# Kernel optimization log

Measured on AMD Instinct MI355X. Metric: run time of the kernel, lower is better.

Reference implementation:

```python
import jax, jax.numpy as jnp
import numpy as np

EPS = float(jnp.finfo(jnp.float32).eps)


def _mlp(x, W1, b1, W2, b2, W3, b3):
    h = jax.nn.relu(x @ W1 + b1)
    h = jax.nn.relu(h @ W2 + b2)
    return h @ W3 + b3


def setup_inputs() -> dict:
    B, D_A, D_B, K, H = 131072, 16, 16, 32, 256
    key = jax.random.key(0)
    ks = jax.random.split(key, 13)
    def lin(k, fi, fo):
        return jax.random.normal(k, (fi, fo), jnp.float32) * (fi ** -0.5)
    inp = {
        "x": jax.random.uniform(ks[0], (B, D_A + D_B), jnp.float32),
        "hW1": lin(ks[1], D_A, H), "hb1": jnp.zeros((H,), jnp.float32),
        "hW2": lin(ks[2], H, H),   "hb2": jnp.zeros((H,), jnp.float32),
        "hW3": lin(ks[3], H, D_B * (K + 1)), "hb3": jnp.zeros((D_B * (K + 1),), jnp.float32),
        "wW1": lin(ks[4], D_A, H), "wb1": jnp.zeros((H,), jnp.float32),
        "wW2": lin(ks[5], H, H),   "wb2": jnp.zeros((H,), jnp.float32),
        "wW3": lin(ks[6], H, D_B * K), "wb3": jnp.zeros((D_B * K,), jnp.float32),
        "A_dims": jnp.arange(0, 32, 2, dtype=jnp.int32),
        "B_dims": jnp.arange(1, 32, 2, dtype=jnp.int32),
    }
    return inp


def reference(x, hW1, hb1, hW2, hb2, hW3, hb3, wW1, wb1, wW2, wb2, wW3, wb3, A_dims, B_dims):
    B = x.shape[0]
    D_B = B_dims.shape[0]
    K = wW3.shape[1] // D_B
    x_A = x[:, A_dims]               # (B, D_A)
    x_B = x[:, B_dims]               # (B, D_B)

    raw_h = _mlp(x_A, hW1, hb1, hW2, hb2, hW3, hb3).reshape(B, D_B, K + 1)
    heights = jax.nn.softplus(raw_h) + EPS
    raw_w = _mlp(x_A, wW1, wb1, wW2, wb2, wW3, wb3).reshape(B, D_B, K)
    widths = jax.nn.softmax(raw_w, axis=-1)
    zeros = jnp.zeros((B, D_B, 1), x.dtype)
    bins = jnp.concatenate([zeros, jnp.cumsum(widths, axis=-1)], axis=-1)  # (B, D_B, K+1)

    # preprocess_params_2: normalise PDF heights and bin areas
    bin_widths = bins[:, :, 1:] - bins[:, :, :-1]
    bin_areas = 0.5 * (heights[:, :, :-1] + heights[:, :, 1:]) * bin_widths  # (B, D_B, K)
    total_area = bin_areas.sum(axis=-1, keepdims=True)
    v = heights / total_area
    bin_areas = bin_areas / total_area

    # bin search
    i = jnp.sum(x_B[..., None] >= bins, axis=-1) - 1
    i = jnp.clip(i, 0, K - 1)                                  # (B, D_B)
    iu = i[..., None]

    x_left = jnp.take_along_axis(bins, iu, axis=2)[..., 0]
    x_right = jnp.take_along_axis(bins, iu + 1, axis=2)[..., 0]
    w_b = x_right - x_left
    v_left = jnp.take_along_axis(v, iu, axis=2)[..., 0]
    v_right = jnp.take_along_axis(v, iu + 1, axis=2)[..., 0]
    w_v = v_right - v_left

    alpha = (x_B - x_left) / (w_b + EPS)
    # cumulative area up to left edge of bin i: exclusive prefix sum then gather
    c_edges = jnp.concatenate([zeros, jnp.cumsum(bin_areas, axis=-1)], axis=-1)
    c_left = jnp.take_along_axis(c_edges, iu, axis=2)[..., 0]

    y_B = c_left + 0.5 * alpha ** 2 * w_v * w_b + alpha * v_left * w_b
    y = x.at[:, B_dims].set(y_B)
    return y
```

## Files before the change

kernel.cpp:

```cpp
#include <hip/hip_runtime.h>
#include <cmath>

typedef short short8 __attribute__((ext_vector_type(8)));
typedef float f32x16 __attribute__((ext_vector_type(16)));

#define EPSF 1.1920929e-07f

#define LDS_XA  0
#define LDS_A1H 3072
#define LDS_A1W 36864
#define LDS_A2H 70656
#define LDS_A2W 104448
#define LDS_H32 3072
#define LDS_TOTAL 138240

#define OFF1H 0
#define OFF1W 4096
#define OFF2H 8192
#define OFF2W 73728
#define OFF3W 139264
#define OFF3H 270336
#define OFFH32 401408

__device__ __forceinline__ unsigned short f2bf(float f) {
  union { float f; unsigned u; } v; v.f = f;
  return (unsigned short)((v.u + 0x8000u) >> 16);
}
__device__ __forceinline__ float sp_eps(float v) {
  return fmaxf(v, 0.f) + __logf(1.f + __expf(-fabsf(v))) + EPSF;
}
__device__ __forceinline__ int chanm(int m) {
  return (((m >> 2) & 1) << 4) + (m & 3) + ((m >> 3) << 2);
}

__global__ void pack_weights(const float* __restrict__ hW1, const float* __restrict__ wW1,
                             const float* __restrict__ hW2, const float* __restrict__ wW2,
                             const float* __restrict__ hW3, const float* __restrict__ wW3,
                             unsigned short* __restrict__ out) {
  int bid = blockIdx.x, l = threadIdx.x;
  int m = l & 31;
  const float* W; unsigned short* dst; int tile, col, NC;
  if (bid < 8)        { W = hW1; dst = out + OFF1H;  tile = bid;       col = tile * 32 + chanm(m); NC = 256; }
  else if (bid < 16)  { W = wW1; dst = out + OFF1W;  tile = bid - 8;   col = tile * 32 + chanm(m); NC = 256; }
  else if (bid < 144) { W = hW2; dst = out + OFF2H;  tile = bid - 16;  col = (tile >> 4) * 32 + chanm(m); NC = 256; }
  else if (bid < 272) { W = wW2; dst = out + OFF2W;  tile = bid - 144; col = (tile >> 4) * 32 + chanm(m); NC = 256; }
  else if (bid < 528) { W = wW3; dst = out + OFF3W;  tile = bid - 272; col = (tile >> 4) * 32 + chanm(m); NC = 512; }
  else if (bid < 784) { W = hW3; dst = out + OFF3H;  tile = bid - 528; col = (tile >> 4) * 33 + chanm(m); NC = 528; }
  else {
    W = hW3; dst = out + OFFH32; tile = bid - 784;
    int q = (m >> 2) & 1, rr = (m & 3) + ((m >> 3) << 2);
    col = q ? -1 : rr * 33 + 32; NC = 528;
  }
  int kt = (bid < 16) ? 0 : (tile & 15);
  int K  = (bid < 16) ? 16 : 256;
  int k0 = kt * 16 + (l >> 5) * 8;
  short8 v;
  #pragma unroll
  for (int e = 0; e < 8; e++) {
    float f = (col >= 0 && (k0 + e) < K) ? W[(k0 + e) * NC + col] : 0.f;
    v[e] = (short)f2bf(f);
  }
  *(short8*)(dst + (tile * 64 + l) * 8) = v;
}

__device__ __forceinline__ void store_relu16(unsigned short* dstRow, f32x16 a) {
  uint4 p0, p1;
  unsigned pk[8];
  #pragma unroll
  for (int j = 0; j < 8; j++) {
    unsigned lo = f2bf(fmaxf(a[2 * j], 0.f));
    unsigned hi = f2bf(fmaxf(a[2 * j + 1], 0.f));
    pk[j] = lo | (hi << 16);
  }
  p0.x = pk[0]; p0.y = pk[1]; p0.z = pk[2]; p0.w = pk[3];
  p1.x = pk[4]; p1.y = pk[5]; p1.z = pk[6]; p1.w = pk[7];
  *(uint4*)(dstRow) = p0;
  *(uint4*)(dstRow + 8) = p1;
}

__global__ __launch_bounds__(1024, 4) void fused_kernel(
    const float* __restrict__ x,
    const float* __restrict__ hb1, const float* __restrict__ hb2, const float* __restrict__ hb3,
    const float* __restrict__ wb1, const float* __restrict__ wb2, const float* __restrict__ wb3,
    const unsigned short* __restrict__ pw,
    float* __restrict__ y) {
  extern __shared__ char lds[];
  const int t = threadIdx.x;
  const int w = t >> 6, l = t & 63, q = l >> 5, r32 = l & 31;
  const int r0 = blockIdx.x * 64;

  unsigned short* XA  = (unsigned short*)(lds + LDS_XA);
  unsigned short* A1H = (unsigned short*)(lds + LDS_A1H);
  unsigned short* A1W = (unsigned short*)(lds + LDS_A1W);
  unsigned short* A2H = (unsigned short*)(lds + LDS_A2H);
  unsigned short* A2W = (unsigned short*)(lds + LDS_A2W);
  float* H32 = (float*)(lds + LDS_H32);

  if (t < 512) {
    int row = t >> 3, c4 = t & 7;
    float4 v = *(const float4*)(x + (r0 + row) * 32 + c4 * 4);
    y[(r0 + row) * 32 + c4 * 4] = v.x;
    y[(r0 + row) * 32 + c4 * 4 + 2] = v.z;
    unsigned short* xa = XA + row * 24 + c4 * 2;
    xa[0] = f2bf(v.x); xa[1] = f2bf(v.z);
  }
  __syncthreads();

  const int net = w >> 3, tc = w & 7;
  unsigned short* A1n = net ? A1W : A1H;
  unsigned short* A2n = net ? A2W : A2H;

  {
    const unsigned short* pA = pw + (net ? OFF1W : OFF1H) + tc * 512;
    const float* b1 = net ? wb1 : hb1;
    f32x16 a0, a1;
    #pragma unroll
    for (int rr = 0; rr < 16; rr++) { float bv = b1[tc * 32 + q * 16 + rr]; a0[rr] = bv; a1[rr] = bv; }
    short8 af = *(const short8*)(pA + l * 8);
    short8 b0 = *(const short8*)(XA + r32 * 24 + q * 8);
    short8 b1f = *(const short8*)(XA + (32 + r32) * 24 + q * 8);
    a0 = __builtin_amdgcn_mfma_f32_32x32x16_bf16(af, b0, a0, 0, 0, 0);
    a1 = __builtin_amdgcn_mfma_f32_32x32x16_bf16(af, b1f, a1, 0, 0, 0);
    store_relu16(A1n + r32 * 264 + tc * 32 + q * 16, a0);
    store_relu16(A1n + (32 + r32) * 264 + tc * 32 + q * 16, a1);
  }
  __syncthreads();

  {
    const unsigned short* pA = pw + (net ? OFF2W : OFF2H) + tc * 16 * 512;
    const float* b2 = net ? wb2 : hb2;
    f32x16 a0, a1;
    #pragma unroll
    for (int rr = 0; rr < 16; rr++) { float bv = b2[tc * 32 + q * 16 + rr]; a0[rr] = bv; a1[rr] = bv; }
    #pragma unroll
    for (int kt = 0; kt < 16; kt++) {
      short8 af = *(const short8*)(pA + kt * 512 + l * 8);
      short8 b0 = *(const short8*)(A1n + r32 * 264 + kt * 16 + q * 8);
      short8 b1f = *(const short8*)(A1n + (32 + r32) * 264 + kt * 16 + q * 8);
      a0 = __builtin_amdgcn_mfma_f32_32x32x16_bf16(af, b0, a0, 0, 0, 0);
      a1 = __builtin_amdgcn_mfma_f32_32x32x16_bf16(af, b1f, a1, 0, 0, 0);
    }
    store_relu16(A2n + r32 * 264 + tc * 32 + q * 16, a0);
    store_relu16(A2n + (32 + r32) * 264 + tc * 32 + q * 16, a1);
  }
  __syncthreads();

  const int d = w;
  f32x16 ew0, ew1, hh0, hh1;
  #pragma unroll
  for (int rr = 0; rr < 16; rr++) {
    float wv = wb3[d * 32 + q * 16 + rr];
    float hv = hb3[d * 33 + q * 16 + rr];
    ew0[rr] = wv; ew1[rr] = wv; hh0[rr] = hv; hh1[rr] = hv;
  }
  {
    const unsigned short* pAW = pw + OFF3W + d * 16 * 512;
    const unsigned short* pAH = pw + OFF3H + d * 16 * 512;
    #pragma unroll
    for (int kt = 0; kt < 16; kt++) {
      short8 aw = *(const short8*)(pAW + kt * 512 + l * 8);
      short8 bw0 = *(const short8*)(A2W + r32 * 264 + kt * 16 + q * 8);
      short8 bw1 = *(const short8*)(A2W + (32 + r32) * 264 + kt * 16 + q * 8);
      ew0 = __builtin_amdgcn_mfma_f32_32x32x16_bf16(aw, bw0, ew0, 0, 0, 0);
      ew1 = __builtin_amdgcn_mfma_f32_32x32x16_bf16(aw, bw1, ew1, 0, 0, 0);
      short8 ah = *(const short8*)(pAH + kt * 512 + l * 8);
      short8 bh0 = *(const short8*)(A2H + r32 * 264 + kt * 16 + q * 8);
      short8 bh1 = *(const short8*)(A2H + (32 + r32) * 264 + kt * 16 + q * 8);
      hh0 = __builtin_amdgcn_mfma_f32_32x32x16_bf16(ah, bh0, hh0, 0, 0, 0);
      hh1 = __builtin_amdgcn_mfma_f32_32x32x16_bf16(ah, bh1, hh1, 0, 0, 0);
    }
  }
  #pragma unroll
  for (int rr = 0; rr < 16; rr++) {
    ew0[rr] = __expf(ew0[rr]); ew1[rr] = __expf(ew1[rr]);
    hh0[rr] = sp_eps(hh0[rr]); hh1[rr] = sp_eps(hh1[rr]);
  }
  if (w >= 14) {
    int rg = w - 14;
    f32x16 a32;
    #pragma unroll
    for (int rr = 0; rr < 16; rr++) a32[rr] = 0.f;
    const unsigned short* pA32 = pw + OFFH32;
    #pragma unroll
    for (int kt = 0; kt < 16; kt++) {
      short8 af = *(const short8*)(pA32 + kt * 512 + l * 8);
      short8 bf = *(const short8*)(A2H + (rg * 32 + r32) * 264 + kt * 16 + q * 8);
      a32 = __builtin_amdgcn_mfma_f32_32x32x16_bf16(af, bf, a32, 0, 0, 0);
    }
    if (q == 0) {
      float* o = H32 + (rg * 32 + r32) * 16;
      #pragma unroll
      for (int g = 0; g < 4; g++) {
        float4 v;
        v.x = sp_eps(a32[g * 4 + 0] + hb3[(g * 4 + 0) * 33 + 32]);
        v.y = sp_eps(a32[g * 4 + 1] + hb3[(g * 4 + 1) * 33 + 32]);
        v.z = sp_eps(a32[g * 4 + 2] + hb3[(g * 4 + 2) * 33 + 32]);
        v.w = sp_eps(a32[g * 4 + 3] + hb3[(g * 4 + 3) * 33 + 32]);
        *(float4*)(o + g * 4) = v;
      }
    }
  }
  __syncthreads();

  #pragma unroll
  for (int rg = 0; rg < 2; rg++) {
    f32x16 e  = rg ? ew1 : ew0;
    f32x16 hh = rg ? hh1 : hh0;
    int row = rg * 32 + r32;
    float se = 0.f;
    #pragma unroll
    for (int k = 0; k < 16; k++) se += e[k];
    float so = __shfl_xor(se, 32);
    float s = se + so;
    float oth0 = __shfl_xor(hh[0], 32);
    float h32v = H32[row * 16 + d];
    float hh16 = q ? h32v : oth0;
    float xbv = x[(r0 + row) * 32 + 2 * d + 1];
    float xbs = xbv * s;
    float bl = q ? so : 0.f;
    int fnd = (xbs >= bl) ? 1 : 0;
    float cl2 = 0.f, sxl = bl, sew = e[0], shl = hh[0], shr = hh[1], scl2 = 0.f;
    #pragma unroll
    for (int k = 0; k < 16; k++) {
      float hn = (k < 15) ? hh[k + 1] : hh16;
      bool c = (xbs >= bl);
      sxl  = c ? bl    : sxl;
      sew  = c ? e[k]  : sew;
      shl  = c ? hh[k] : shl;
      shr  = c ? hn    : shr;
      scl2 = c ? cl2   : scl2;
      cl2 += (hh[k] + hn) * e[k];
      bl  += e[k];
    }
    float cl2o = __shfl_xor(cl2, 32);
    float S2 = cl2 + cl2o;
    if (q) scl2 += cl2o;
    int   o_fnd  = __shfl_xor(fnd, 32);
    float o_sxl  = __shfl_xor(sxl, 32);
    float o_sew  = __shfl_xor(sew, 32);
    float o_shl  = __shfl_xor(shl, 32);
    float o_shr  = __shfl_xor(shr, 32);
    float o_scl2 = __shfl_xor(scl2, 32);
    bool other = q ? (fnd == 0) : (o_fnd != 0);
    float gsxl  = other ? o_sxl  : sxl;
    float gsew  = other ? o_sew  : sew;
    float gshl  = other ? o_shl  : shl;
    float gshr  = other ? o_shr  : shr;
    float gscl2 = other ? o_scl2 : scl2;
    float alpha = (xbs - gsxl) / (gsew + EPSF);
    float yv = (gscl2 + (alpha * alpha * (gshr - gshl) + 2.f * alpha * gshl) * gsew) / S2;
    if (q == 0) y[(r0 + row) * 32 + 2 * d + 1] = yv;
  }
}

extern "C" void kernel_launch(void* const* d_in, const int* in_sizes, int n_in,
                              void* d_out, int out_size, void* d_ws, size_t ws_size,
                              hipStream_t stream) {
  const float* x   = (const float*)d_in[0];
  const float* hW1 = (const float*)d_in[1];
  const float* hb1 = (const float*)d_in[2];
  const float* hW2 = (const float*)d_in[3];
  const float* hb2 = (const float*)d_in[4];
  const float* hW3 = (const float*)d_in[5];
  const float* hb3 = (const float*)d_in[6];
  const float* wW1 = (const float*)d_in[7];
  const float* wb1 = (const float*)d_in[8];
  const float* wW2 = (const float*)d_in[9];
  const float* wb2 = (const float*)d_in[10];
  const float* wW3 = (const float*)d_in[11];
  const float* wb3 = (const float*)d_in[12];
  unsigned short* pw = (unsigned short*)d_ws;

  pack_weights<<<800, 64, 0, stream>>>(hW1, wW1, hW2, wW2, hW3, wW3, pw);

  hipFuncSetAttribute((const void*)fused_kernel,
                      hipFuncAttributeMaxDynamicSharedMemorySize, LDS_TOTAL);
  fused_kernel<<<2048, 1024, LDS_TOTAL, stream>>>(
      x, hb1, hb2, hb3, wb1, wb2, wb3, pw, (float*)d_out);
}
```

Baseline: 199.5 us.

## Halve block to 512 threads with wider per-wave MFMA tiles and LDS exp exchange

Cuts the workgroup from 16 to 8 waves. Each wave now computes two output column tiles in layers 1 and 2 and four output dims in layer 3, so every B-operand load from LDS is reused across more MFMAs. Waves for the width net write bf16 exp values into LDS, and the height-net waves read them back to run the spline evaluation. This reduces LDS operand traffic and the number of waves per block, at the cost of more accumulator registers per wave, bf16 rounding of the exp weights, and half the waves sitting idle during the final stage.

```diff
diff --git a/kernel.cpp b/kernel.cpp
--- a/kernel.cpp
+++ b/kernel.cpp
@@ -9,9 +9,10 @@
 #define LDS_XA  0
 #define LDS_A1H 3072
 #define LDS_A1W 36864
-#define LDS_A2H 70656
-#define LDS_A2W 104448
-#define LDS_H32 3072
+#define LDS_A2W 70656
+#define LDS_A2H 104448
+#define LDS_EW  0
+#define LDS_H32 66560
 #define LDS_TOTAL 138240
 
 #define OFF1H 0
@@ -25,6 +26,12 @@
 __device__ __forceinline__ unsigned short f2bf(float f) {
   union { float f; unsigned u; } v; v.f = f;
   return (unsigned short)((v.u + 0x8000u) >> 16);
+}
+__device__ __forceinline__ float bf_lo(unsigned u) {
+  union { unsigned u; float f; } v; v.u = u << 16; return v.f;
+}
+__device__ __forceinline__ float bf_hi(unsigned u) {
+  union { unsigned u; float f; } v; v.u = u & 0xffff0000u; return v.f;
 }
 __device__ __forceinline__ float sp_eps(float v) {
   return fmaxf(v, 0.f) + __logf(1.f + __expf(-fabsf(v))) + EPSF;
@@ -63,8 +70,7 @@
   *(short8*)(dst + (tile * 64 + l) * 8) = v;
 }
 
-__device__ __forceinline__ void store_relu16(unsigned short* dstRow, f32x16 a) {
-  uint4 p0, p1;
+__device__ __forceinline__ void store_relu16(unsigned short* dst, f32x16 a) {
   unsigned pk[8];
   #pragma unroll
   for (int j = 0; j < 8; j++) {
@@ -72,13 +78,24 @@
     unsigned hi = f2bf(fmaxf(a[2 * j + 1], 0.f));
     pk[j] = lo | (hi << 16);
   }
-  p0.x = pk[0]; p0.y = pk[1]; p0.z = pk[2]; p0.w = pk[3];
-  p1.x = pk[4]; p1.y = pk[5]; p1.z = pk[6]; p1.w = pk[7];
-  *(uint4*)(dstRow) = p0;
-  *(uint4*)(dstRow + 8) = p1;
-}
-
-__global__ __launch_bounds__(1024, 4) void fused_kernel(
+  uint4 p0 = {pk[0], pk[1], pk[2], pk[3]}, p1 = {pk[4], pk[5], pk[6], pk[7]};
+  *(uint4*)(dst) = p0;
+  *(uint4*)(dst + 8) = p1;
+}
+__device__ __forceinline__ void store_exp16(unsigned short* dst, f32x16 a) {
+  unsigned pk[8];
+  #pragma unroll
+  for (int j = 0; j < 8; j++) {
+    unsigned lo = f2bf(__expf(a[2 * j]));
+    unsigned hi = f2bf(__expf(a[2 * j + 1]));
+    pk[j] = lo | (hi << 16);
+  }
+  uint4 p0 = {pk[0], pk[1], pk[2], pk[3]}, p1 = {pk[4], pk[5], pk[6], pk[7]};
+  *(uint4*)(dst) = p0;
+  *(uint4*)(dst + 8) = p1;
+}
+
+__global__ __launch_bounds__(512, 2) void fused_kernel(
     const float* __restrict__ x,
     const float* __restrict__ hb1, const float* __restrict__ hb2, const float* __restrict__ hb3,
     const float* __restrict__ wb1, const float* __restrict__ wb2, const float* __restrict__ wb3,
@@ -94,9 +111,10 @@
   unsigned short* A1W = (unsigned short*)(lds + LDS_A1W);
   unsigned short* A2H = (unsigned short*)(lds + LDS_A2H);
   unsigned short* A2W = (unsigned short*)(lds + LDS_A2W);
-  float* H32 = (float*)(lds + LDS_H32);
-
-  if (t < 512) {
+  unsigned short* EWp = (unsigned short*)(lds + LDS_EW);
+  float* H32p = (float*)(lds + LDS_H32);
+
+  {
     int row = t >> 3, c4 = t & 7;
     float4 v = *(const float4*)(x + (r0 + row) * 32 + c4 * 4);
     y[(r0 + row) * 32 + c4 * 4] = v.x;
@@ -106,150 +124,188 @@
   }
   __syncthreads();
 
-  const int net = w >> 3, tc = w & 7;
-  unsigned short* A1n = net ? A1W : A1H;
-  unsigned short* A2n = net ? A2W : A2H;
-
-  {
-    const unsigned short* pA = pw + (net ? OFF1W : OFF1H) + tc * 512;
-    const float* b1 = net ? wb1 : hb1;
-    f32x16 a0, a1;
-    #pragma unroll
-    for (int rr = 0; rr < 16; rr++) { float bv = b1[tc * 32 + q * 16 + rr]; a0[rr] = bv; a1[rr] = bv; }
-    short8 af = *(const short8*)(pA + l * 8);
-    short8 b0 = *(const short8*)(XA + r32 * 24 + q * 8);
-    short8 b1f = *(const short8*)(XA + (32 + r32) * 24 + q * 8);
-    a0 = __builtin_amdgcn_mfma_f32_32x32x16_bf16(af, b0, a0, 0, 0, 0);
-    a1 = __builtin_amdgcn_mfma_f32_32x32x16_bf16(af, b1f, a1, 0, 0, 0);
-    store_relu16(A1n + r32 * 264 + tc * 32 + q * 16, a0);
-    store_relu16(A1n + (32 + r32) * 264 + tc * 32 + q * 16, a1);
+  const int netH = (w >= 4);
+  const int tcp = (w & 3) * 2;
+  unsigned short* A1n = netH ? A1H : A1W;
+  unsigned short* A2n = netH ? A2H : A2W;
+
+  {
+    const float* b1 = netH ? hb1 : wb1;
+    const unsigned short* base = pw + (netH ? OFF1H : OFF1W);
+    short8 xb0 = *(const short8*)(XA + r32 * 24 + q * 8);
+    short8 xb1 = *(const short8*)(XA + (32 + r32) * 24 + q * 8);
+    #pragma unroll
+    for (int tt = 0; tt < 2; tt++) {
+      int tc = tcp + tt;
+      f32x16 a0, a1;
+      #pragma unroll
+      for (int rr = 0; rr < 16; rr++) { float bv = b1[tc * 32 + q * 16 + rr]; a0[rr] = bv; a1[rr] = bv; }
+      short8 af = *(const short8*)(base + tc * 512 + l * 8);
+      a0 = __builtin_amdgcn_mfma_f32_32x32x16_bf16(af, xb0, a0, 0, 0, 0);
+      a1 = __builtin_amdgcn_mfma_f32_32x32x16_bf16(af, xb1, a1, 0, 0, 0);
+      store_relu16(A1n + r32 * 264 + tc * 32 + q * 16, a0);
+      store_relu16(A1n + (32 + r32) * 264 + tc * 32 + q * 16, a1);
+    }
   }
   __syncthreads();
 
   {
-    const unsigned short* pA = pw + (net ? OFF2W : OFF2H) + tc * 16 * 512;
-    const float* b2 = net ? wb2 : hb2;
-    f32x16 a0, a1;
-    #pragma unroll
-    for (int rr = 0; rr < 16; rr++) { float bv = b2[tc * 32 + q * 16 + rr]; a0[rr] = bv; a1[rr] = bv; }
+    const float* b2 = netH ? hb2 : wb2;
+    const unsigned short* aB = pw + (netH ? OFF2H : OFF2W);
+    f32x16 a00, a01, a10, a11;
+    #pragma unroll
+    for (int rr = 0; rr < 16; rr++) {
+      float b0v = b2[tcp * 32 + q * 16 + rr];
+      float b1v = b2[(tcp + 1) * 32 + q * 16 + rr];
+      a00[rr] = b0v; a01[rr] = b0v; a10[rr] = b1v; a11[rr] = b1v;
+    }
     #pragma unroll
     for (int kt = 0; kt < 16; kt++) {
-      short8 af = *(const short8*)(pA + kt * 512 + l * 8);
       short8 b0 = *(const short8*)(A1n + r32 * 264 + kt * 16 + q * 8);
-      short8 b1f = *(const short8*)(A1n + (32 + r32) * 264 + kt * 16 + q * 8);
-      a0 = __builtin_amdgcn_mfma_f32_32x32x16_bf16(af, b0, a0, 0, 0, 0);
-      a1 = __builtin_amdgcn_mfma_f32_32x32x16_bf16(af, b1f, a1, 0, 0, 0);
-    }
-    store_relu16(A2n + r32 * 264 + tc * 32 + q * 16, a0);
-    store_relu16(A2n + (32 + r32) * 264 + tc * 32 + q * 16, a1);
+      short8 b1 = *(const short8*)(A1n + (32 + r32) * 264 + kt * 16 + q * 8);
+      short8 af0 = *(const short8*)(aB + (tcp * 16 + kt) * 512 + l * 8);
+      short8 af1 = *(const short8*)(aB + ((tcp + 1) * 16 + kt) * 512 + l * 8);
+      a00 = __builtin_amdgcn_mfma_f32_32x32x16_bf16(af0, b0, a00, 0, 0, 0);
+      a01 = __builtin_amdgcn_mfma_f32_32x32x16_bf16(af0, b1, a01, 0, 0, 0);
+      a10 = __builtin_amdgcn_mfma_f32_32x32x16_bf16(af1, b0, a10, 0, 0, 0);
+      a11 = __builtin_amdgcn_mfma_f32_32x32x16_bf16(af1, b1, a11, 0, 0, 0);
+    }
+    store_relu16(A2n + r32 * 264 + tcp * 32 + q * 16, a00);
+    store_relu16(A2n + (32 + r32) * 264 + tcp * 32 + q * 16, a01);
+    store_relu16(A2n + r32 * 264 + (tcp + 1) * 32 + q * 16, a10);
+    store_relu16(A2n + (32 + r32) * 264 + (tcp + 1) * 32 + q * 16, a11);
   }
   __syncthreads();
 
-  const int d = w;
-  f32x16 ew0, ew1, hh0, hh1;
+  const int db = (w & 3) * 4;
+  f32x16 acc[4][2];
+  {
+    const float* b3 = netH ? hb3 : wb3;
+    #pragma unroll
+    for (int dd = 0; dd < 4; dd++) {
+      #pragma unroll
+      for (int rr = 0; rr < 16; rr++) {
+        float bv = netH ? b3[(db + dd) * 33 + q * 16 + rr] : b3[(db + dd) * 32 + q * 16 + rr];
+        acc[dd][0][rr] = bv; acc[dd][1][rr] = bv;
+      }
+    }
+  }
+  f32x16 acc32;
   #pragma unroll
-  for (int rr = 0; rr < 16; rr++) {
-    float wv = wb3[d * 32 + q * 16 + rr];
-    float hv = hb3[d * 33 + q * 16 + rr];
-    ew0[rr] = wv; ew1[rr] = wv; hh0[rr] = hv; hh1[rr] = hv;
-  }
-  {
-    const unsigned short* pAW = pw + OFF3W + d * 16 * 512;
-    const unsigned short* pAH = pw + OFF3H + d * 16 * 512;
+  for (int rr = 0; rr < 16; rr++) acc32[rr] = 0.f;
+  {
+    const unsigned short* aB3 = pw + (netH ? OFF3H : OFF3W);
     #pragma unroll
     for (int kt = 0; kt < 16; kt++) {
-      short8 aw = *(const short8*)(pAW + kt * 512 + l * 8);
-      short8 bw0 = *(const short8*)(A2W + r32 * 264 + kt * 16 + q * 8);
-      short8 bw1 = *(const short8*)(A2W + (32 + r32) * 264 + kt * 16 + q * 8);
-      ew0 = __builtin_amdgcn_mfma_f32_32x32x16_bf16(aw, bw0, ew0, 0, 0, 0);
-      ew1 = __builtin_amdgcn_mfma_f32_32x32x16_bf16(aw, bw1, ew1, 0, 0, 0);
-      short8 ah = *(const short8*)(pAH + kt * 512 + l * 8);
-      short8 bh0 = *(const short8*)(A2H + r32 * 264 + kt * 16 + q * 8);
-      short8 bh1 = *(const short8*)(A2H + (32 + r32) * 264 + kt * 16 + q * 8);
-      hh0 = __builtin_amdgcn_mfma_f32_32x32x16_bf16(ah, bh0, hh0, 0, 0, 0);
-      hh1 = __builtin_amdgcn_mfma_f32_32x32x16_bf16(ah, bh1, hh1, 0, 0, 0);
-    }
-  }
-  #pragma unroll
-  for (int rr = 0; rr < 16; rr++) {
-    ew0[rr] = __expf(ew0[rr]); ew1[rr] = __expf(ew1[rr]);
-    hh0[rr] = sp_eps(hh0[rr]); hh1[rr] = sp_eps(hh1[rr]);
-  }
-  if (w >= 14) {
-    int rg = w - 14;
-    f32x16 a32;
-    #pragma unroll
-    for (int rr = 0; rr < 16; rr++) a32[rr] = 0.f;
-    const unsigned short* pA32 = pw + OFFH32;
-    #pragma unroll
-    for (int kt = 0; kt < 16; kt++) {
-      short8 af = *(const short8*)(pA32 + kt * 512 + l * 8);
-      short8 bf = *(const short8*)(A2H + (rg * 32 + r32) * 264 + kt * 16 + q * 8);
-      a32 = __builtin_amdgcn_mfma_f32_32x32x16_bf16(af, bf, a32, 0, 0, 0);
-    }
-    if (q == 0) {
-      float* o = H32 + (rg * 32 + r32) * 16;
+      short8 b0 = *(const short8*)(A2n + r32 * 264 + kt * 16 + q * 8);
+      short8 b1 = *(const short8*)(A2n + (32 + r32) * 264 + kt * 16 + q * 8);
+      #pragma unroll
+      for (int dd = 0; dd < 4; dd++) {
+        short8 af = *(const short8*)(aB3 + ((db + dd) * 16 + kt) * 512 + l * 8);
+        acc[dd][0] = __builtin_amdgcn_mfma_f32_32x32x16_bf16(af, b0, acc[dd][0], 0, 0, 0);
+        acc[dd][1] = __builtin_amdgcn_mfma_f32_32x32x16_bf16(af, b1, acc[dd][1], 0, 0, 0);
+      }
+      if (w >= 6) {
+        short8 af32 = *(const short8*)(pw + OFFH32 + kt * 512 + l * 8);
+        acc32 = __builtin_amdgcn_mfma_f32_32x32x16_bf16(af32, (w == 6) ? b0 : b1, acc32, 0, 0, 0);
+      }
+    }
+  }
+  if (!netH) {
+    #pragma unroll
+    for (int dd = 0; dd < 4; dd++)
+      #pragma unroll
+      for (int rg = 0; rg < 2; rg++)
+        store_exp16(EWp + (rg * 32 + r32) * 520 + (db + dd) * 32 + q * 16, acc[dd][rg]);
+  } else {
+    #pragma unroll
+    for (int dd = 0; dd < 4; dd++)
+      #pragma unroll
+      for (int rg = 0; rg < 2; rg++)
+        #pragma unroll
+        for (int rr = 0; rr < 16; rr++)
+          acc[dd][rg][rr] = sp_eps(acc[dd][rg][rr]);
+    if (w >= 6 && q == 0) {
+      int rgg = w - 6;
+      float* o = H32p + (rgg * 32 + r32) * 16;
       #pragma unroll
       for (int g = 0; g < 4; g++) {
         float4 v;
-        v.x = sp_eps(a32[g * 4 + 0] + hb3[(g * 4 + 0) * 33 + 32]);
-        v.y = sp_eps(a32[g * 4 + 1] + hb3[(g * 4 + 1) * 33 + 32]);
-        v.z = sp_eps(a32[g * 4 + 2] + hb3[(g * 4 + 2) * 33 + 32]);
-        v.w = sp_eps(a32[g * 4 + 3] + hb3[(g * 4 + 3) * 33 + 32]);
+        v.x = sp_eps(acc32[g * 4 + 0] + hb3[(g * 4 + 0) * 33 + 32]);
+        v.y = sp_eps(acc32[g * 4 + 1] + hb3[(g * 4 + 1) * 33 + 32]);
+        v.z = sp_eps(acc32[g * 4 + 2] + hb3[(g * 4 + 2) * 33 + 32]);
+        v.w = sp_eps(acc32[g * 4 + 3] + hb3[(g * 4 + 3) * 33 + 32]);
         *(float4*)(o + g * 4) = v;
       }
     }
   }
   __syncthreads();
 
-  #pragma unroll
-  for (int rg = 0; rg < 2; rg++) {
-    f32x16 e  = rg ? ew1 : ew0;
-    f32x16 hh = rg ? hh1 : hh0;
-    int row = rg * 32 + r32;
-    float se = 0.f;
-    #pragma unroll
-    for (int k = 0; k < 16; k++) se += e[k];
-    float so = __shfl_xor(se, 32);
-    float s = se + so;
-    float oth0 = __shfl_xor(hh[0], 32);
-    float h32v = H32[row * 16 + d];
-    float hh16 = q ? h32v : oth0;
-    float xbv = x[(r0 + row) * 32 + 2 * d + 1];
-    float xbs = xbv * s;
-    float bl = q ? so : 0.f;
-    int fnd = (xbs >= bl) ? 1 : 0;
-    float cl2 = 0.f, sxl = bl, sew = e[0], shl = hh[0], shr = hh[1], scl2 = 0.f;
-    #pragma unroll
-    for (int k = 0; k < 16; k++) {
-      float hn = (k < 15) ? hh[k + 1] : hh16;
-      bool c = (xbs >= bl);
-      sxl  = c ? bl    : sxl;
-      sew  = c ? e[k]  : sew;
-      shl  = c ? hh[k] : shl;
-      shr  = c ? hn    : shr;
-      scl2 = c ? cl2   : scl2;
-      cl2 += (hh[k] + hn) * e[k];
-      bl  += e[k];
-    }
-    float cl2o = __shfl_xor(cl2, 32);
-    float S2 = cl2 + cl2o;
-    if (q) scl2 += cl2o;
-    int   o_fnd  = __shfl_xor(fnd, 32);
-    float o_sxl  = __shfl_xor(sxl, 32);
-    float o_sew  = __shfl_xor(sew, 32);
-    float o_shl  = __shfl_xor(shl, 32);
-    float o_shr  = __shfl_xor(shr, 32);
-    float o_scl2 = __shfl_xor(scl2, 32);
-    bool other = q ? (fnd == 0) : (o_fnd != 0);
-    float gsxl  = other ? o_sxl  : sxl;
-    float gsew  = other ? o_sew  : sew;
-    float gshl  = other ? o_shl  : shl;
-    float gshr  = other ? o_shr  : shr;
-    float gscl2 = other ? o_scl2 : scl2;
-    float alpha = (xbs - gsxl) / (gsew + EPSF);
-    float yv = (gscl2 + (alpha * alpha * (gshr - gshl) + 2.f * alpha * gshl) * gsew) / S2;
-    if (q == 0) y[(r0 + row) * 32 + 2 * d + 1] = yv;
+  if (netH) {
+    #pragma unroll
+    for (int dd = 0; dd < 4; dd++) {
+      #pragma unroll
+      for (int rg = 0; rg < 2; rg++) {
+        f32x16 hh = acc[dd][rg];
+        int d = db + dd, row = rg * 32 + r32, grow = r0 + row;
+        const unsigned short* ep = EWp + row * 520 + d * 32 + q * 16;
+        uint4 ev0 = *(const uint4*)(ep);
+        uint4 ev1 = *(const uint4*)(ep + 8);
+        float e[16];
+        e[0] = bf_lo(ev0.x);  e[1] = bf_hi(ev0.x);
+        e[2] = bf_lo(ev0.y);  e[3] = bf_hi(ev0.y);
+        e[4] = bf_lo(ev0.z);  e[5] = bf_hi(ev0.z);
+        e[6] = bf_lo(ev0.w);  e[7] = bf_hi(ev0.w);
+        e[8] = bf_lo(ev1.x);  e[9] = bf_hi(ev1.x);
+        e[10] = bf_lo(ev1.y); e[11] = bf_hi(ev1.y);
+        e[12] = bf_lo(ev1.z); e[13] = bf_hi(ev1.z);
+        e[14] = bf_lo(ev1.w); e[15] = bf_hi(ev1.w);
+        float se = 0.f;
+        #pragma unroll
+        for (int k = 0; k < 16; k++) se += e[k];
+        float so = __shfl_xor(se, 32);
+        float s = se + so;
+        float h16 = __shfl_xor(hh[0], 32);
+        float h32v = H32p[row * 16 + d];
+        float hlast = q ? h32v : h16;
+        float xbv = x[grow * 32 + 2 * d + 1];
+        float xbs = xbv * s;
+        float bl = q ? so : 0.f;
+        int fnd = (xbs >= bl) ? 1 : 0;
+        float cl2 = 0.f, sxl = bl, sew = e[0], shl = hh[0], shr = hh[1], scl2 = 0.f;
+        #pragma unroll
+        for (int k = 0; k < 16; k++) {
+          float hk = hh[k];
+          float hn = (k < 15) ? hh[k + 1] : hlast;
+          bool c = (xbs >= bl);
+          sxl  = c ? bl   : sxl;
+          sew  = c ? e[k] : sew;
+          shl  = c ? hk   : shl;
+          shr  = c ? hn   : shr;
+          scl2 = c ? cl2  : scl2;
+          cl2 += (hk + hn) * e[k];
+          bl  += e[k];
+        }
+        float cl2o = __shfl_xor(cl2, 32);
+        float S2 = cl2 + cl2o;
+        scl2 += q ? cl2o : 0.f;
+        int   o_fnd  = __shfl_xor(fnd, 32);
+        float o_sxl  = __shfl_xor(sxl, 32);
+        float o_sew  = __shfl_xor(sew, 32);
+        float o_shl  = __shfl_xor(shl, 32);
+        float o_shr  = __shfl_xor(shr, 32);
+        float o_scl2 = __shfl_xor(scl2, 32);
+        bool other = q ? (fnd == 0) : (o_fnd != 0);
+        float gsxl  = other ? o_sxl  : sxl;
+        float gsew  = other ? o_sew  : sew;
+        float gshl  = other ? o_shl  : shl;
+        float gshr  = other ? o_shr  : shr;
+        float gscl2 = other ? o_scl2 : scl2;
+        float alpha = (xbs - gsxl) / (gsew + EPSF);
+        float yv = (gscl2 + (alpha * alpha * (gshr - gshl) + 2.f * alpha * gshl) * gsew) / S2;
+        if (q == 0) y[grow * 32 + 2 * d + 1] = yv;
+      }
+    }
   }
 }
 
@@ -275,6 +331,6 @@
 
   hipFuncSetAttribute((const void*)fused_kernel,
                       hipFuncAttributeMaxDynamicSharedMemorySize, LDS_TOTAL);
-  fused_kernel<<<2048, 1024, LDS_TOTAL, stream>>>(
+  fused_kernel<<<2048, 512, LDS_TOTAL, stream>>>(
       x, hb1, hb2, hb3, wb1, wb2, wb3, pw, (float*)d_out);
 }
```

New measurement: 232.4 us. 16.5% more time.

## Shrink blocks to 32 rows with 8 waves, reuse LDS buffers, raise occupancy

Applied to the files above, without the earlier changes.

Each block now covers 32 rows with 512 threads instead of 64 rows with 1024. The two networks' layer-2 GEMMs run one after the other so LDS buffers can be reused, cutting LDS from about 138KB to 52KB and allowing more resident blocks per CU. The output stage loops over two groups of 8 dims per wave instead of holding four accumulators, which reduces register pressure. It also adds a packed bf16 convert instruction, vectorized bias loads, and a pre-reordered hb3 bias written by an extra pack block. In exchange there are more barriers and each wave now performs its layer-2 and layer-3 GEMMs one after the other instead of interleaved.

```diff
diff --git a/kernel.cpp b/kernel.cpp
--- a/kernel.cpp
+++ b/kernel.cpp
@@ -6,13 +6,11 @@
 
 #define EPSF 1.1920929e-07f
 
-#define LDS_XA  0
-#define LDS_A1H 3072
-#define LDS_A1W 36864
-#define LDS_A2H 70656
-#define LDS_A2W 104448
-#define LDS_H32 3072
-#define LDS_TOTAL 138240
+#define LDS_XA 0
+#define LDS_X1 1536
+#define LDS_X2 18432
+#define LDS_X3 35328
+#define LDS_TOTAL 52224
 
 #define OFF1H 0
 #define OFF1W 4096
@@ -21,6 +19,7 @@
 #define OFF3W 139264
 #define OFF3H 270336
 #define OFFH32 401408
+#define OFFB_BYTES 819200
 
 __device__ __forceinline__ unsigned short f2bf(float f) {
   union { float f; unsigned u; } v; v.f = f;
@@ -32,12 +31,27 @@
 __device__ __forceinline__ int chanm(int m) {
   return (((m >> 2) & 1) << 4) + (m & 3) + ((m >> 3) << 2);
 }
+__device__ __forceinline__ unsigned cvtpk(float lo, float hi) {
+  unsigned r;
+  asm("v_cvt_pk_bf16_f32 %0, %1, %2" : "=v"(r) : "v"(lo), "v"(hi));
+  return r;
+}
 
 __global__ void pack_weights(const float* __restrict__ hW1, const float* __restrict__ wW1,
                              const float* __restrict__ hW2, const float* __restrict__ wW2,
                              const float* __restrict__ hW3, const float* __restrict__ wW3,
+                             const float* __restrict__ hb3,
                              unsigned short* __restrict__ out) {
   int bid = blockIdx.x, l = threadIdx.x;
+  if (bid == 800) {
+    float* fb = (float*)((char*)out + OFFB_BYTES);
+    for (int idx = l; idx < 528; idx += 64) {
+      int d = idx / 33, j = idx - d * 33;
+      if (j < 32) fb[d * 32 + j] = hb3[idx];
+      else fb[512 + d] = hb3[idx];
+    }
+    return;
+  }
   int m = l & 31;
   const float* W; unsigned short* dst; int tile, col, NC;
   if (bid < 8)        { W = hW1; dst = out + OFF1H;  tile = bid;       col = tile * 32 + chanm(m); NC = 256; }
@@ -48,8 +62,8 @@
   else if (bid < 784) { W = hW3; dst = out + OFF3H;  tile = bid - 528; col = (tile >> 4) * 33 + chanm(m); NC = 528; }
   else {
     W = hW3; dst = out + OFFH32; tile = bid - 784;
-    int q = (m >> 2) & 1, rr = (m & 3) + ((m >> 3) << 2);
-    col = q ? -1 : rr * 33 + 32; NC = 528;
+    int qq = (m >> 2) & 1, rr = (m & 3) + ((m >> 3) << 2);
+    col = qq ? -1 : rr * 33 + 32; NC = 528;
   }
   int kt = (bid < 16) ? 0 : (tile & 15);
   int K  = (bid < 16) ? 16 : 256;
@@ -63,40 +77,114 @@
   *(short8*)(dst + (tile * 64 + l) * 8) = v;
 }
 
-__device__ __forceinline__ void store_relu16(unsigned short* dstRow, f32x16 a) {
-  uint4 p0, p1;
-  unsigned pk[8];
-  #pragma unroll
-  for (int j = 0; j < 8; j++) {
-    unsigned lo = f2bf(fmaxf(a[2 * j], 0.f));
-    unsigned hi = f2bf(fmaxf(a[2 * j + 1], 0.f));
-    pk[j] = lo | (hi << 16);
-  }
-  p0.x = pk[0]; p0.y = pk[1]; p0.z = pk[2]; p0.w = pk[3];
-  p1.x = pk[4]; p1.y = pk[5]; p1.z = pk[6]; p1.w = pk[7];
-  *(uint4*)(dstRow) = p0;
-  *(uint4*)(dstRow + 8) = p1;
-}
-
-__global__ __launch_bounds__(1024, 4) void fused_kernel(
+__device__ __forceinline__ f32x16 bias_init(const float* __restrict__ b) {
+  const float4* bp = (const float4*)b;
+  float4 b0 = bp[0], b1 = bp[1], b2 = bp[2], b3 = bp[3];
+  f32x16 a;
+  a[0] = b0.x;  a[1] = b0.y;  a[2] = b0.z;  a[3] = b0.w;
+  a[4] = b1.x;  a[5] = b1.y;  a[6] = b1.z;  a[7] = b1.w;
+  a[8] = b2.x;  a[9] = b2.y;  a[10] = b2.z; a[11] = b2.w;
+  a[12] = b3.x; a[13] = b3.y; a[14] = b3.z; a[15] = b3.w;
+  return a;
+}
+
+__device__ __forceinline__ void store_act16(unsigned short* dst, f32x16 a) {
+  unsigned pk0 = cvtpk(fmaxf(a[0], 0.f),  fmaxf(a[1], 0.f));
+  unsigned pk1 = cvtpk(fmaxf(a[2], 0.f),  fmaxf(a[3], 0.f));
+  unsigned pk2 = cvtpk(fmaxf(a[4], 0.f),  fmaxf(a[5], 0.f));
+  unsigned pk3 = cvtpk(fmaxf(a[6], 0.f),  fmaxf(a[7], 0.f));
+  unsigned pk4 = cvtpk(fmaxf(a[8], 0.f),  fmaxf(a[9], 0.f));
+  unsigned pk5 = cvtpk(fmaxf(a[10], 0.f), fmaxf(a[11], 0.f));
+  unsigned pk6 = cvtpk(fmaxf(a[12], 0.f), fmaxf(a[13], 0.f));
+  unsigned pk7 = cvtpk(fmaxf(a[14], 0.f), fmaxf(a[15], 0.f));
+  uint4 p0 = {pk0, pk1, pk2, pk3}, p1 = {pk4, pk5, pk6, pk7};
+  *(uint4*)dst = p0;
+  *(uint4*)(dst + 8) = p1;
+}
+
+__device__ __forceinline__ void l2_phase(const unsigned short* __restrict__ src,
+                                         unsigned short* __restrict__ dst,
+                                         const unsigned short* __restrict__ aBase,
+                                         const float* __restrict__ bias,
+                                         int w, int l, int q, int r32) {
+  f32x16 acc = bias_init(bias + w * 32 + q * 16);
+  const unsigned short* aB = aBase + w * 16 * 512 + l * 8;
+  const unsigned short* bB = src + r32 * 264 + q * 8;
+  #pragma unroll
+  for (int kt = 0; kt < 16; kt++)
+    acc = __builtin_amdgcn_mfma_f32_32x32x16_bf16(*(const short8*)(aB + kt * 512),
+                                                  *(const short8*)(bB + kt * 16), acc, 0, 0, 0);
+  store_act16(dst + r32 * 264 + w * 32 + q * 16, acc);
+}
+
+__device__ __forceinline__ void spline_store(f32x16 e, f32x16 hh, int d, int r32, int q,
+                                             const float* __restrict__ H32p,
+                                             const float* __restrict__ x,
+                                             float* __restrict__ y, int r0) {
+  int grow = r0 + r32;
+  float se = 0.f;
+  #pragma unroll
+  for (int k = 0; k < 16; k++) se += e[k];
+  float so = __shfl_xor(se, 32);
+  float s = se + so;
+  float h16o = __shfl_xor(hh[0], 32);
+  float hlast = q ? H32p[r32 * 16 + d] : h16o;
+  float xbv = x[grow * 32 + 2 * d + 1];
+  float xbs = xbv * s;
+  float bl0 = q ? so : 0.f;
+  int fnd = (xbs >= bl0) ? 1 : 0;
+  float bl = bl0, cl2 = 0.f, sxl = bl0, sew = e[0], shl = hh[0], shr = hh[1], scl2 = 0.f;
+  #pragma unroll
+  for (int k = 0; k < 16; k++) {
+    float hk = hh[k];
+    float hn = (k < 15) ? hh[k + 1] : hlast;
+    bool c = (xbs >= bl);
+    sxl  = c ? bl   : sxl;
+    sew  = c ? e[k] : sew;
+    shl  = c ? hk   : shl;
+    shr  = c ? hn   : shr;
+    scl2 = c ? cl2  : scl2;
+    cl2 += (hk + hn) * e[k];
+    bl  += e[k];
+  }
+  float cl2o = __shfl_xor(cl2, 32);
+  float S2 = cl2 + cl2o;
+  scl2 += q ? cl2o : 0.f;
+  int   o_fnd  = __shfl_xor(fnd, 32);
+  float o_sxl  = __shfl_xor(sxl, 32);
+  float o_sew  = __shfl_xor(sew, 32);
+  float o_shl  = __shfl_xor(shl, 32);
+  float o_shr  = __shfl_xor(shr, 32);
+  float o_scl2 = __shfl_xor(scl2, 32);
+  bool other = q ? (fnd == 0) : (o_fnd != 0);
+  float gsxl  = other ? o_sxl  : sxl;
+  float gsew  = other ? o_sew  : sew;
+  float gshl  = other ? o_shl  : shl;
+  float gshr  = other ? o_shr  : shr;
+  float gscl2 = other ? o_scl2 : scl2;
+  float alpha = (xbs - gsxl) / (gsew + EPSF);
+  float yv = (gscl2 + (alpha * alpha * (gshr - gshl) + 2.f * alpha * gshl) * gsew) / S2;
+  if (q == 0) y[grow * 32 + 2 * d + 1] = yv;
+}
+
+__global__ __launch_bounds__(512, 6) void fused_kernel(
     const float* __restrict__ x,
-    const float* __restrict__ hb1, const float* __restrict__ hb2, const float* __restrict__ hb3,
-    const float* __restrict__ wb1, const float* __restrict__ wb2, const float* __restrict__ wb3,
+    const float* __restrict__ hb1, const float* __restrict__ hb2,
+    const float* __restrict__ wb1, const float* __restrict__ wb2,
+    const float* __restrict__ wb3,
     const unsigned short* __restrict__ pw,
     float* __restrict__ y) {
   extern __shared__ char lds[];
   const int t = threadIdx.x;
   const int w = t >> 6, l = t & 63, q = l >> 5, r32 = l & 31;
-  const int r0 = blockIdx.x * 64;
-
-  unsigned short* XA  = (unsigned short*)(lds + LDS_XA);
-  unsigned short* A1H = (unsigned short*)(lds + LDS_A1H);
-  unsigned short* A1W = (unsigned short*)(lds + LDS_A1W);
-  unsigned short* A2H = (unsigned short*)(lds + LDS_A2H);
-  unsigned short* A2W = (unsigned short*)(lds + LDS_A2W);
-  float* H32 = (float*)(lds + LDS_H32);
-
-  if (t < 512) {
+  const int r0 = blockIdx.x * 32;
+
+  unsigned short* XA = (unsigned short*)(lds + LDS_XA);
+  unsigned short* X1 = (unsigned short*)(lds + LDS_X1);
+  unsigned short* X2 = (unsigned short*)(lds + LDS_X2);
+  unsigned short* X3 = (unsigned short*)(lds + LDS_X3);
+
+  if (t < 256) {
     int row = t >> 3, c4 = t & 7;
     float4 v = *(const float4*)(x + (r0 + row) * 32 + c4 * 4);
     y[(r0 + row) * 32 + c4 * 4] = v.x;
@@ -106,150 +194,77 @@
   }
   __syncthreads();
 
-  const int net = w >> 3, tc = w & 7;
-  unsigned short* A1n = net ? A1W : A1H;
-  unsigned short* A2n = net ? A2W : A2H;
-
   {
-    const unsigned short* pA = pw + (net ? OFF1W : OFF1H) + tc * 512;
-    const float* b1 = net ? wb1 : hb1;
-    f32x16 a0, a1;
+    short8 bx = *(const short8*)(XA + r32 * 24 + q * 8);
+    f32x16 ah = bias_init(hb1 + w * 32 + q * 16);
+    ah = __builtin_amdgcn_mfma_f32_32x32x16_bf16(
+        *(const short8*)(pw + OFF1H + w * 512 + l * 8), bx, ah, 0, 0, 0);
+    store_act16(X1 + r32 * 264 + w * 32 + q * 16, ah);
+    f32x16 aw = bias_init(wb1 + w * 32 + q * 16);
+    aw = __builtin_amdgcn_mfma_f32_32x32x16_bf16(
+        *(const short8*)(pw + OFF1W + w * 512 + l * 8), bx, aw, 0, 0, 0);
+    store_act16(X2 + r32 * 264 + w * 32 + q * 16, aw);
+  }
+  __syncthreads();
+
+  l2_phase(X1, X3, pw + OFF2H, hb2, w, l, q, r32);
+  __syncthreads();
+  l2_phase(X2, X1, pw + OFF2W, wb2, w, l, q, r32);
+  __syncthreads();
+
+  const float* pwf = (const float*)((const char*)pw + OFFB_BYTES);
+  const float* H32p = (const float*)(lds + LDS_X2);
+  #pragma unroll 1
+  for (int p = 0; p < 2; p++) {
+    const int d = p * 8 + w;
+    f32x16 e = bias_init(wb3 + d * 32 + q * 16);
+    {
+      const unsigned short* aW = pw + OFF3W + d * 16 * 512 + l * 8;
+      const unsigned short* bW = X1 + r32 * 264 + q * 8;
+      #pragma unroll
+      for (int kt = 0; kt < 16; kt++)
+        e = __builtin_amdgcn_mfma_f32_32x32x16_bf16(*(const short8*)(aW + kt * 512),
+                                                    *(const short8*)(bW + kt * 16), e, 0, 0, 0);
+    }
     #pragma unroll
-    for (int rr = 0; rr < 16; rr++) { float bv = b1[tc * 32 + q * 16 + rr]; a0[rr] = bv; a1[rr] = bv; }
-    short8 af = *(const short8*)(pA + l * 8);
-    short8 b0 = *(const short8*)(XA + r32 * 24 + q * 8);
-    short8 b1f = *(const short8*)(XA + (32 + r32) * 24 + q * 8);
-    a0 = __builtin_amdgcn_mfma_f32_32x32x16_bf16(af, b0, a0, 0, 0, 0);
-    a1 = __builtin_amdgcn_mfma_f32_32x32x16_bf16(af, b1f, a1, 0, 0, 0);
-    store_relu16(A1n + r32 * 264 + tc * 32 + q * 16, a0);
-    store_relu16(A1n + (32 + r32) * 264 + tc * 32 + q * 16, a1);
-  }
-  __syncthreads();
-
-  {
-    const unsigned short* pA = pw + (net ? OFF2W : OFF2H) + tc * 16 * 512;
-    const float* b2 = net ? wb2 : hb2;
-    f32x16 a0, a1;
+    for (int rr = 0; rr < 16; rr++) e[rr] = __expf(e[rr]);
+    f32x16 hh = bias_init(pwf + d * 32 + q * 16);
+    {
+      const unsigned short* aH = pw + OFF3H + d * 16 * 512 + l * 8;
+      const unsigned short* bH = X3 + r32 * 264 + q * 8;
+      #pragma unroll
+      for (int kt = 0; kt < 16; kt++)
+        hh = __builtin_amdgcn_mfma_f32_32x32x16_bf16(*(const short8*)(aH + kt * 512),
+                                                     *(const short8*)(bH + kt * 16), hh, 0, 0, 0);
+    }
     #pragma unroll
-    for (int rr = 0; rr < 16; rr++) { float bv = b2[tc * 32 + q * 16 + rr]; a0[rr] = bv; a1[rr] = bv; }
-    #pragma unroll
-    for (int kt = 0; kt < 16; kt++) {
-      short8 af = *(const short8*)(pA + kt * 512 + l * 8);
-      short8 b0 = *(const short8*)(A1n + r32 * 264 + kt * 16 + q * 8);
-      short8 b1f = *(const short8*)(A1n + (32 + r32) * 264 + kt * 16 + q * 8);
-      a0 = __builtin_amdgcn_mfma_f32_32x32x16_bf16(af, b0, a0, 0, 0, 0);
-      a1 = __builtin_amdgcn_mfma_f32_32x32x16_bf16(af, b1f, a1, 0, 0, 0);
-    }
-    store_relu16(A2n + r32 * 264 + tc * 32 + q * 16, a0);
-    store_relu16(A2n + (32 + r32) * 264 + tc * 32 + q * 16, a1);
-  }
-  __syncthreads();
-
-  const int d = w;
-  f32x16 ew0, ew1, hh0, hh1;
-  #pragma unroll
-  for (int rr = 0; rr < 16; rr++) {
-    float wv = wb3[d * 32 + q * 16 + rr];
-    float hv = hb3[d * 33 + q * 16 + rr];
-    ew0[rr] = wv; ew1[rr] = wv; hh0[rr] = hv; hh1[rr] = hv;
-  }
-  {
-    const unsigned short* pAW = pw + OFF3W + d * 16 * 512;
-    const unsigned short* pAH = pw + OFF3H + d * 16 * 512;
-    #pragma unroll
-    for (int kt = 0; kt < 16; kt++) {
-      short8 aw = *(const short8*)(pAW + kt * 512 + l * 8);
-      short8 bw0 = *(const short8*)(A2W + r32 * 264 + kt * 16 + q * 8);
-      short8 bw1 = *(const short8*)(A2W + (32 + r32) * 264 + kt * 16 + q * 8);
-      ew0 = __builtin_amdgcn_mfma_f32_32x32x16_bf16(aw, bw0, ew0, 0, 0, 0);
-      ew1 = __builtin_amdgcn_mfma_f32_32x32x16_bf16(aw, bw1, ew1, 0, 0, 0);
-      short8 ah = *(const short8*)(pAH + kt * 512 + l * 8);
-      short8 bh0 = *(const short8*)(A2H + r32 * 264 + kt * 16 + q * 8);
-      short8 bh1 = *(const short8*)(A2H + (32 + r32) * 264 + kt * 16 + q * 8);
-      hh0 = __builtin_amdgcn_mfma_f32_32x32x16_bf16(ah, bh0, hh0, 0, 0, 0);
-      hh1 = __builtin_amdgcn_mfma_f32_32x32x16_bf16(ah, bh1, hh1, 0, 0, 0);
-    }
-  }
-  #pragma unroll
-  for (int rr = 0; rr < 16; rr++) {
-    ew0[rr] = __expf(ew0[rr]); ew1[rr] = __expf(ew1[rr]);
-    hh0[rr] = sp_eps(hh0[rr]); hh1[rr] = sp_eps(hh1[rr]);
-  }
-  if (w >= 14) {
-    int rg = w - 14;
-    f32x16 a32;
-    #pragma unroll
-    for (int rr = 0; rr < 16; rr++) a32[rr] = 0.f;
-    const unsigned short* pA32 = pw + OFFH32;
-    #pragma unroll
-    for (int kt = 0; kt < 16; kt++) {
-      short8 af = *(const short8*)(pA32 + kt * 512 + l * 8);
-      short8 bf = *(const short8*)(A2H + (rg * 32 + r32) * 264 + kt * 16 + q * 8);
-      a32 = __builtin_amdgcn_mfma_f32_32x32x16_bf16(af, bf, a32, 0, 0, 0);
-    }
-    if (q == 0) {
-      float* o = H32 + (rg * 32 + r32) * 16;
-      #pragma unroll
-      for (int g = 0; g < 4; g++) {
-        float4 v;
-        v.x = sp_eps(a32[g * 4 + 0] + hb3[(g * 4 + 0) * 33 + 32]);
-        v.y = sp_eps(a32[g * 4 + 1] + hb3[(g * 4 + 1) * 33 + 32]);
-        v.z = sp_eps(a32[g * 4 + 2] + hb3[(g * 4 + 2) * 33 + 32]);
-        v.w = sp_eps(a32[g * 4 + 3] + hb3[(g * 4 + 3) * 33 + 32]);
-        *(float4*)(o + g * 4) = v;
+    for (int rr = 0; rr < 16; rr++) hh[rr] = sp_eps(hh[rr]);
+    if (p == 0 && w == 7) {
+      f32x16 a32;
+      #pragma unroll
+      for (int rr = 0; rr < 16; rr++) a32[rr] = 0.f;
+      const unsigned short* a32p = pw + OFFH32 + l * 8;
+      const unsigned short* bH = X3 + r32 * 264 + q * 8;
+      #pragma unroll
+      for (int kt = 0; kt < 16; kt++)
+        a32 = __builtin_amdgcn_mfma_f32_32x32x16_bf16(*(const short8*)(a32p + kt * 512),
+                                                      *(const short8*)(bH + kt * 16), a32, 0, 0, 0);
+      if (q == 0) {
+        float* o = (float*)(lds + LDS_X2) + r32 * 16;
+        const float* hb32 = pwf + 512;
+        #pragma unroll
+        for (int g = 0; g < 4; g++) {
+          float4 v;
+          v.x = sp_eps(a32[4 * g + 0] + hb32[4 * g + 0]);
+          v.y = sp_eps(a32[4 * g + 1] + hb32[4 * g + 1]);
+          v.z = sp_eps(a32[4 * g + 2] + hb32[4 * g + 2]);
+          v.w = sp_eps(a32[4 * g + 3] + hb32[4 * g + 3]);
+          *(float4*)(o + 4 * g) = v;
+        }
       }
     }
-  }
-  __syncthreads();
-
-  #pragma unroll
-  for (int rg = 0; rg < 2; rg++) {
-    f32x16 e  = rg ? ew1 : ew0;
-    f32x16 hh = rg ? hh1 : hh0;
-    int row = rg * 32 + r32;
-    float se = 0.f;
-    #pragma unroll
-    for (int k = 0; k < 16; k++) se += e[k];
-    float so = __shfl_xor(se, 32);
-    float s = se + so;
-    float oth0 = __shfl_xor(hh[0], 32);
-    float h32v = H32[row * 16 + d];
-    float hh16 = q ? h32v : oth0;
-    float xbv = x[(r0 + row) * 32 + 2 * d + 1];
-    float xbs = xbv * s;
-    float bl = q ? so : 0.f;
-    int fnd = (xbs >= bl) ? 1 : 0;
-    float cl2 = 0.f, sxl = bl, sew = e[0], shl = hh[0], shr = hh[1], scl2 = 0.f;
-    #pragma unroll
-    for (int k = 0; k < 16; k++) {
-      float hn = (k < 15) ? hh[k + 1] : hh16;
-      bool c = (xbs >= bl);
-      sxl  = c ? bl    : sxl;
-      sew  = c ? e[k]  : sew;
-      shl  = c ? hh[k] : shl;
-      shr  = c ? hn    : shr;
-      scl2 = c ? cl2   : scl2;
-      cl2 += (hh[k] + hn) * e[k];
-      bl  += e[k];
-    }
-    float cl2o = __shfl_xor(cl2, 32);
-    float S2 = cl2 + cl2o;
-    if (q) scl2 += cl2o;
-    int   o_fnd  = __shfl_xor(fnd, 32);
-    float o_sxl  = __shfl_xor(sxl, 32);
-    float o_sew  = __shfl_xor(sew, 32);
-    float o_shl  = __shfl_xor(shl, 32);
-    float o_shr  = __shfl_xor(shr, 32);
-    float o_scl2 = __shfl_xor(scl2, 32);
-    bool other = q ? (fnd == 0) : (o_fnd != 0);
-    float gsxl  = other ? o_sxl  : sxl;
-    float gsew  = other ? o_sew  : sew;
-    float gshl  = other ? o_shl  : shl;
-    float gshr  = other ? o_shr  : shr;
-    float gscl2 = other ? o_scl2 : scl2;
-    float alpha = (xbs - gsxl) / (gsew + EPSF);
-    float yv = (gscl2 + (alpha * alpha * (gshr - gshl) + 2.f * alpha * gshl) * gsew) / S2;
-    if (q == 0) y[(r0 + row) * 32 + 2 * d + 1] = yv;
+    if (p == 0) __syncthreads();
+    spline_store(e, hh, d, r32, q, H32p, x, y, r0);
   }
 }
 
@@ -271,10 +286,10 @@
   const float* wb3 = (const float*)d_in[12];
   unsigned short* pw = (unsigned short*)d_ws;
 
-  pack_weights<<<800, 64, 0, stream>>>(hW1, wW1, hW2, wW2, hW3, wW3, pw);
+  pack_weights<<<801, 64, 0, stream>>>(hW1, wW1, hW2, wW2, hW3, wW3, hb3, pw);
 
   hipFuncSetAttribute((const void*)fused_kernel,
                       hipFuncAttributeMaxDynamicSharedMemorySize, LDS_TOTAL);
-  fused_kernel<<<2048, 1024, LDS_TOTAL, stream>>>(
-      x, hb1, hb2, hb3, wb1, wb2, wb3, pw, (float*)d_out);
-}
+  fused_kernel<<<4096, 512, LDS_TOTAL, stream>>>(
+      x, hb1, hb2, wb1, wb2, wb3, pw, (float*)d_out);
+}
```

New measurement: 355.9 us. 1.78x slower.
